# Optimization experiments

Hardware: AMD Instinct MI355X
Metric: run time of the kernel (lower is better)

The kernel has to match this reference:

```python
import jax, jax.numpy as jnp
import numpy as np
from jax import lax

B, T, D, N = 64, 4096, 256, 64


def setup_inputs() -> dict:
    key = jax.random.key(0)
    ks = jax.random.split(key, 3)
    return {
        "x": jax.random.normal(ks[0], (B, T, D), dtype=jnp.float32),
        "mask": jnp.ones((B, T), dtype=bool),
        "W": jax.random.normal(ks[1], (D, N), dtype=jnp.float32) * (1.0 / np.sqrt(D)),
        "b": jnp.zeros((N,), dtype=jnp.float32),
        "trans": jax.random.normal(ks[2], (N, N), dtype=jnp.float32) * 0.1,
        "left_boundary": jnp.zeros((N,), dtype=jnp.float32),
        "right_boundary": jnp.zeros((N,), dtype=jnp.float32),
    }


def _viterbi_decode(potentials, lens, trans):
    # potentials: [B, T, N]; lens: [B] int32; trans: [N, N]
    Tt = potentials.shape[1]

    def fwd_step(state, inp):
        pot_t, t = inp  # pot_t: [B, N], t scalar time index (1..T-1)
        scores = state[:, :, None] + trans[None, :, :]        # [B, N_prev, N_cur]
        bp = jnp.argmax(scores, axis=1).astype(jnp.int32)      # [B, N]
        new_state = pot_t + jnp.max(scores, axis=1)            # [B, N]
        valid = (t < lens)[:, None]                            # carry state past length
        return jnp.where(valid, new_state, state), bp

    pots_t = jnp.swapaxes(potentials, 0, 1)  # [T, B, N]
    final_state, bps = lax.scan(fwd_step, pots_t[0], (pots_t[1:], jnp.arange(1, Tt)))
    last_tag = jnp.argmax(final_state, axis=1).astype(jnp.int32)  # [B]

    def bwd_step(tag, inp):
        bp, t = inp  # bp: [B, N] backpointers for time t+1; t in 0..T-2
        prev = jnp.take_along_axis(bp, tag[:, None], axis=1)[:, 0]
        new_tag = jnp.where(t < lens - 1, prev, last_tag)
        return new_tag, new_tag

    _, tags = lax.scan(bwd_step, last_tag, (bps, jnp.arange(Tt - 1)), reverse=True)
    # tags: [T-1, B], position t holds decoded tag at time t
    decoded = jnp.concatenate([tags.T, last_tag[:, None]], axis=1)  # [B, T]
    return decoded


def reference(x, mask, W, b, trans, left_boundary, right_boundary):
    # projection (use_kernel=True)
    pot = jnp.einsum("btd,dn->btn", x, W) + b  # [B, T, N]
    # boundary potentials (use_boundary=True): added at fixed first/last timestep
    pot = pot.at[:, 0, :].add(left_boundary)
    pot = pot.at[:, -1, :].add(right_boundary)
    lens = jnp.sum(mask.astype(jnp.int32), axis=1)  # [B]
    decoded = _viterbi_decode(pot, lens, trans)
    return decoded, pot, lens, trans
```

## Files before the change

### kernel.cpp

```cpp
#include <hip/hip_runtime.h>

#define B_ 64
#define T_ 4096
#define D_ 256
#define N_ 64

typedef float f32x16 __attribute__((ext_vector_type(16)));

__global__ __launch_bounds__(64) void k_misc(const unsigned char* __restrict__ mask,
                                             const float* __restrict__ trans,
                                             float* __restrict__ out_lens,
                                             float* __restrict__ out_trans,
                                             int* __restrict__ lens_i) {
  int blk = blockIdx.x, lane = threadIdx.x;
  if (blk < B_) {
    int probe = (int)mask[0] + (int)mask[1] + (int)mask[2] + (int)mask[3];
    int cnt = 0;
    if (probe >= 2) {
      const unsigned char* row = mask + (size_t)blk * T_;
      for (int i = lane; i < T_; i += 64) cnt += row[i] ? 1 : 0;
    } else {
      const int* rowi = (const int*)mask + (size_t)blk * T_;
      for (int i = lane; i < T_; i += 64) cnt += rowi[i] ? 1 : 0;
    }
    #pragma unroll
    for (int off = 32; off > 0; off >>= 1) cnt += __shfl_down(cnt, off, 64);
    if (lane == 0) { out_lens[blk] = (float)cnt; lens_i[blk] = cnt; }
  } else {
    int base = (blk - B_) * 1024;
    for (int i = lane; i < 1024; i += 64) out_trans[base + i] = trans[base + i];
  }
}

__global__ __launch_bounds__(256, 4) void k_gemm(const float* __restrict__ x,
                                                 const float* __restrict__ W,
                                                 const float* __restrict__ bias,
                                                 const float* __restrict__ lb,
                                                 const float* __restrict__ rb,
                                                 float* __restrict__ pot) {
  int wave = (blockIdx.x * blockDim.x + threadIdx.x) >> 6;
  int wave_u = __builtin_amdgcn_readfirstlane(wave);
  int lane = threadIdx.x & 63;
  long row0 = (long)wave_u * 16;

  float bv = bias[lane];
  float lbv = lb[lane];
  float rbv = rb[lane];

  float acc[16];
  #pragma unroll
  for (int r = 0; r < 16; ++r) {
    int t = (int)((row0 + r) & (T_ - 1));
    float a = bv;
    if (t == 0)      a += lbv;
    if (t == T_ - 1) a += rbv;
    acc[r] = a;
  }

  const float* xb = x + (size_t)row0 * D_;

  #pragma unroll
  for (int c = 0; c < 4; ++c) {
    int d0 = c * 64;
    float w[64];
    #pragma unroll
    for (int k = 0; k < 64; ++k) w[k] = W[(d0 + k) * N_ + lane];
    #pragma unroll
    for (int r = 0; r < 16; ++r) {
      const f32x16* xr = reinterpret_cast<const f32x16*>(xb + r * D_ + d0);
      #pragma unroll
      for (int q = 0; q < 4; ++q) {
        f32x16 xv = xr[q];
        #pragma unroll
        for (int j = 0; j < 16; ++j) acc[r] += xv[j] * w[q * 16 + j];
      }
    }
  }

  #pragma unroll
  for (int r = 0; r < 16; ++r) pot[(row0 + r) * N_ + lane] = acc[r];
}

#define FWD_STEP(TIDX, PREG)                                                      \
  {                                                                               \
    float pot_t = PREG;                                                           \
    int tp = (TIDX) + 4; if (tp > T_ - 1) tp = T_ - 1;                            \
    PREG = pb[(size_t)tp * N_ + lane];                                            \
    float m[64];                                                                  \
    _Pragma("unroll")                                                             \
    for (int g = 0; g < 16; ++g) {                                                \
      float4 s4 = st4v[g];                                                        \
      float2 ca = make_float2(s4.x, s4.y) + t2[2 * g];                            \
      float2 cb = make_float2(s4.z, s4.w) + t2[2 * g + 1];                        \
      m[4 * g + 0] = ca.x; m[4 * g + 1] = ca.y;                                   \
      m[4 * g + 2] = cb.x; m[4 * g + 3] = cb.y;                                   \
    }                                                                             \
    float r1[22];                                                                 \
    _Pragma("unroll")                                                             \
    for (int i = 0; i < 21; ++i)                                                  \
      r1[i] = fmaxf(fmaxf(m[3 * i], m[3 * i + 1]), m[3 * i + 2]);                 \
    r1[21] = m[63];                                                               \
    float r2[8];                                                                  \
    _Pragma("unroll")                                                             \
    for (int i = 0; i < 7; ++i)                                                   \
      r2[i] = fmaxf(fmaxf(r1[3 * i], r1[3 * i + 1]), r1[3 * i + 2]);              \
    r2[7] = r1[21];                                                               \
    float r3a = fmaxf(fmaxf(r2[0], r2[1]), r2[2]);                                \
    float r3b = fmaxf(fmaxf(r2[3], r2[4]), r2[5]);                                \
    float r3c = fmaxf(r2[6], r2[7]);                                              \
    float best = fmaxf(fmaxf(r3a, r3b), r3c);                                     \
    float ns = pot_t + best;                                                      \
    state = ((TIDX) < len_b) ? ns : state;                                        \
    sb[(size_t)(TIDX) * N_ + lane] = state;                                       \
    __builtin_amdgcn_wave_barrier();                                              \
    st[lane] = state;                                                             \
    __builtin_amdgcn_wave_barrier();                                              \
  }

__global__ __launch_bounds__(64, 1) void k_fwd_states(const float* __restrict__ pot,
                                                      const float* __restrict__ trans,
                                                      const int* __restrict__ lens_i,
                                                      float* __restrict__ states,
                                                      float* __restrict__ fstate) {
  int b = blockIdx.x, lane = threadIdx.x;
  __shared__ float4 st4v[16];
  float* st = (float*)st4v;

  float2 t2[32];
  #pragma unroll
  for (int p = 0; p < 32; ++p)
    t2[p] = make_float2(trans[(2 * p) * N_ + lane], trans[(2 * p + 1) * N_ + lane]);

  const float* pb = pot + (size_t)b * T_ * N_;
  float* sb = states + (size_t)b * T_ * N_;
  int len_b = lens_i[b];

  float state = pb[lane];
  st[lane] = state;
  sb[lane] = state;
  __builtin_amdgcn_wave_barrier();

  float p0 = pb[1 * N_ + lane];
  float p1 = pb[2 * N_ + lane];
  float p2 = pb[3 * N_ + lane];
  float p3 = pb[4 * N_ + lane];

  int t = 1;
  for (; t + 3 <= T_ - 1; t += 4) {
    FWD_STEP(t + 0, p0);
    FWD_STEP(t + 1, p1);
    FWD_STEP(t + 2, p2);
    FWD_STEP(t + 3, p3);
  }
  FWD_STEP(t + 0, p0);
  FWD_STEP(t + 1, p1);
  FWD_STEP(t + 2, p2);

  fstate[b * N_ + lane] = state;
}

#define BP_CHUNK 64
__global__ __launch_bounds__(64, 2) void k_bp(const float* __restrict__ states,
                                              const float* __restrict__ trans,
                                              unsigned char* __restrict__ bp) {
  int nchunk = T_ / BP_CHUNK;
  int b = blockIdx.x / nchunk;
  int chunk = blockIdx.x - b * nchunk;
  int lane = threadIdx.x;

  float tcol[64];
  #pragma unroll
  for (int p = 0; p < 64; ++p) tcol[p] = trans[p * N_ + lane];

  int t0 = chunk * BP_CHUNK;
  int tstart = (t0 == 0) ? 1 : t0;
  int tend = t0 + BP_CHUNK;

  for (int t = tstart; t < tend; ++t) {
    const f32x16* sr = reinterpret_cast<const f32x16*>(states + ((size_t)b * T_ + (t - 1)) * N_);
    f32x16 s0 = sr[0], s1 = sr[1], s2 = sr[2], s3 = sr[3];

    float c[64];
    #pragma unroll
    for (int j = 0; j < 16; ++j) {
      c[j]      = s0[j] + tcol[j];
      c[16 + j] = s1[j] + tcol[16 + j];
      c[32 + j] = s2[j] + tcol[32 + j];
      c[48 + j] = s3[j] + tcol[48 + j];
    }

    float r1[22];
    #pragma unroll
    for (int i = 0; i < 21; ++i) r1[i] = fmaxf(fmaxf(c[3 * i], c[3 * i + 1]), c[3 * i + 2]);
    r1[21] = c[63];
    float r2[8];
    #pragma unroll
    for (int i = 0; i < 7; ++i) r2[i] = fmaxf(fmaxf(r1[3 * i], r1[3 * i + 1]), r1[3 * i + 2]);
    r2[7] = r1[21];
    float r3a = fmaxf(fmaxf(r2[0], r2[1]), r2[2]);
    float r3b = fmaxf(fmaxf(r2[3], r2[4]), r2[5]);
    float r3c = fmaxf(r2[6], r2[7]);
    float best = fmaxf(fmaxf(r3a, r3b), r3c);

    int bpi = 63;
    #pragma unroll
    for (int p = 62; p >= 0; --p) bpi = (c[p] == best) ? p : bpi;

    bp[((size_t)b * T_ + t) * N_ + lane] = (unsigned char)bpi;
  }
}

__global__ __launch_bounds__(64, 1) void k_bwd(const unsigned char* __restrict__ bp,
                                               const float* __restrict__ fstate,
                                               const int* __restrict__ lens_i,
                                               float* __restrict__ decoded) {
  int b = blockIdx.x, lane = threadIdx.x;

  __shared__ float fv[64];
  __shared__ int sh_tag;
  fv[lane] = fstate[b * N_ + lane];
  __syncthreads();
  if (lane == 0) {
    float best = fv[0]; int tg = 0;
    for (int i = 1; i < 64; ++i) if (fv[i] > best) { best = fv[i]; tg = i; }
    sh_tag = tg;
  }
  __syncthreads();
  int last_tag = sh_tag;
  int len_b = lens_i[b];

  const unsigned char* bpb = bp + (size_t)b * T_ * N_;
  float* dec = decoded + (size_t)b * T_;

  int tag = last_tag;
  if (lane == 0) dec[T_ - 1] = (float)last_tag;

  const int G = 16;
  int bufA[G], bufB[G];
  const int k0 = T_ - 1;
  #pragma unroll
  for (int i = 0; i < G; ++i) bufA[i] = (int)bpb[(size_t)(k0 - i) * N_ + lane];

  const int nrows = T_ - 1;
  const int groups = nrows / G;

  for (int g = 0; g < groups; ++g) {
    int kn = k0 - G * (g + 1);
    #pragma unroll
    for (int i = 0; i < G; ++i)
      bufB[i] = (kn - i >= 1) ? (int)bpb[(size_t)(kn - i) * N_ + lane] : 0;

    int kbase = k0 - G * g;
    #pragma unroll
    for (int i = 0; i < G; ++i) {
      int k = kbase - i;
      int prev = __shfl(bufA[i], tag, 64);
      int t = k - 1;
      tag = (t < len_b - 1) ? prev : last_tag;
      if (lane == 0) dec[t] = (float)tag;
    }
    #pragma unroll
    for (int i = 0; i < G; ++i) bufA[i] = bufB[i];
  }

  int kbase = k0 - G * groups;
  #pragma unroll
  for (int i = 0; i < G; ++i) {
    int k = kbase - i;
    if (k >= 1) {
      int prev = __shfl(bufA[i], tag, 64);
      int t = k - 1;
      tag = (t < len_b - 1) ? prev : last_tag;
      if (lane == 0) dec[t] = (float)tag;
    }
  }
}

extern "C" void kernel_launch(void* const* d_in, const int* in_sizes, int n_in,
                              void* d_out, int out_size, void* d_ws, size_t ws_size,
                              hipStream_t stream) {
  const float* x            = (const float*)d_in[0];
  const unsigned char* mask = (const unsigned char*)d_in[1];
  const float* W            = (const float*)d_in[2];
  const float* bias         = (const float*)d_in[3];
  const float* trans        = (const float*)d_in[4];
  const float* lb           = (const float*)d_in[5];
  const float* rb           = (const float*)d_in[6];

  float* out         = (float*)d_out;
  float* out_decoded = out;
  float* out_pot     = out + (size_t)B_ * T_;
  float* out_lens    = out_pot + (size_t)B_ * T_ * N_;
  float* out_trans   = out_lens + B_;

  const size_t bp_bytes     = (size_t)B_ * T_ * N_;
  const size_t fstate_off   = bp_bytes;
  const size_t lens_off     = fstate_off + (size_t)B_ * N_ * 4;
  const size_t states_off   = lens_off + 256;
  const size_t states_bytes = (size_t)B_ * T_ * N_ * 4;

  unsigned char* bp = (unsigned char*)d_ws;
  float* fstate     = (float*)((char*)d_ws + fstate_off);
  int*   lens_i     = (int*)((char*)d_ws + lens_off);
  float* states     = (float*)((char*)d_ws + states_off);

  k_misc<<<68, 64, 0, stream>>>(mask, trans, out_lens, out_trans, lens_i);
  k_gemm<<<(B_ * T_) / 64, 256, 0, stream>>>(x, W, bias, lb, rb, out_pot);
  k_fwd_states<<<B_, 64, 0, stream>>>(out_pot, trans, lens_i, states, fstate);
  k_bp<<<B_ * (T_ / BP_CHUNK), 64, 0, stream>>>(states, trans, bp);
  k_bwd<<<B_, 64, 0, stream>>>(bp, fstate, lens_i, out_decoded);
}
```

Before: 1.759 ms.

## Broadcast Viterbi state via readlane instead of LDS; deepen prefetch and scalarize backtrace

The forward recurrence now takes each previous-state value with readlane from the register holding it, in place of writing state to LDS and reading it back between wave barriers. This removes the per-step LDS round trip and barriers from the serial critical path, though it issues 64 readlanes per step. The pot prefetch distance grows from 4 to 8 timesteps. The backtrace holds the tag in a scalar and uses readlane instead of ds_bpermute shuffles, with a larger group of 32 buffered rows.

```diff
diff --git a/kernel.cpp b/kernel.cpp
--- a/kernel.cpp
+++ b/kernel.cpp
@@ -84,16 +84,14 @@
 #define FWD_STEP(TIDX, PREG)                                                      \
   {                                                                               \
     float pot_t = PREG;                                                           \
-    int tp = (TIDX) + 4; if (tp > T_ - 1) tp = T_ - 1;                            \
+    int tp = (TIDX) + 8; if (tp > T_ - 1) tp = T_ - 1;                            \
     PREG = pb[(size_t)tp * N_ + lane];                                            \
     float m[64];                                                                  \
     _Pragma("unroll")                                                             \
-    for (int g = 0; g < 16; ++g) {                                                \
-      float4 s4 = st4v[g];                                                        \
-      float2 ca = make_float2(s4.x, s4.y) + t2[2 * g];                            \
-      float2 cb = make_float2(s4.z, s4.w) + t2[2 * g + 1];                        \
-      m[4 * g + 0] = ca.x; m[4 * g + 1] = ca.y;                                   \
-      m[4 * g + 2] = cb.x; m[4 * g + 3] = cb.y;                                   \
+    for (int p = 0; p < 64; ++p) {                                                \
+      float sp = __int_as_float(                                                  \
+          __builtin_amdgcn_readlane(__float_as_int(state), p));                   \
+      m[p] = sp + tcol[p];                                                        \
     }                                                                             \
     float r1[22];                                                                 \
     _Pragma("unroll")                                                             \
@@ -112,9 +110,6 @@
     float ns = pot_t + best;                                                      \
     state = ((TIDX) < len_b) ? ns : state;                                        \
     sb[(size_t)(TIDX) * N_ + lane] = state;                                       \
-    __builtin_amdgcn_wave_barrier();                                              \
-    st[lane] = state;                                                             \
-    __builtin_amdgcn_wave_barrier();                                              \
   }
 
 __global__ __launch_bounds__(64, 1) void k_fwd_states(const float* __restrict__ pot,
@@ -123,38 +118,45 @@
                                                       float* __restrict__ states,
                                                       float* __restrict__ fstate) {
   int b = blockIdx.x, lane = threadIdx.x;
-  __shared__ float4 st4v[16];
-  float* st = (float*)st4v;
-
-  float2 t2[32];
-  #pragma unroll
-  for (int p = 0; p < 32; ++p)
-    t2[p] = make_float2(trans[(2 * p) * N_ + lane], trans[(2 * p + 1) * N_ + lane]);
+
+  float tcol[64];
+  #pragma unroll
+  for (int p = 0; p < 64; ++p) tcol[p] = trans[p * N_ + lane];
 
   const float* pb = pot + (size_t)b * T_ * N_;
   float* sb = states + (size_t)b * T_ * N_;
   int len_b = lens_i[b];
 
   float state = pb[lane];
-  st[lane] = state;
   sb[lane] = state;
-  __builtin_amdgcn_wave_barrier();
 
   float p0 = pb[1 * N_ + lane];
   float p1 = pb[2 * N_ + lane];
   float p2 = pb[3 * N_ + lane];
   float p3 = pb[4 * N_ + lane];
+  float p4 = pb[5 * N_ + lane];
+  float p5 = pb[6 * N_ + lane];
+  float p6 = pb[7 * N_ + lane];
+  float p7 = pb[8 * N_ + lane];
 
   int t = 1;
-  for (; t + 3 <= T_ - 1; t += 4) {
+  for (; t + 7 <= T_ - 1; t += 8) {
     FWD_STEP(t + 0, p0);
     FWD_STEP(t + 1, p1);
     FWD_STEP(t + 2, p2);
     FWD_STEP(t + 3, p3);
+    FWD_STEP(t + 4, p4);
+    FWD_STEP(t + 5, p5);
+    FWD_STEP(t + 6, p6);
+    FWD_STEP(t + 7, p7);
   }
   FWD_STEP(t + 0, p0);
   FWD_STEP(t + 1, p1);
   FWD_STEP(t + 2, p2);
+  FWD_STEP(t + 3, p3);
+  FWD_STEP(t + 4, p4);
+  FWD_STEP(t + 5, p5);
+  FWD_STEP(t + 6, p6);
 
   fstate[b * N_ + lane] = state;
 }
@@ -226,16 +228,16 @@
     sh_tag = tg;
   }
   __syncthreads();
-  int last_tag = sh_tag;
+  int s_last = __builtin_amdgcn_readfirstlane(sh_tag);
   int len_b = lens_i[b];
 
   const unsigned char* bpb = bp + (size_t)b * T_ * N_;
   float* dec = decoded + (size_t)b * T_;
 
-  int tag = last_tag;
-  if (lane == 0) dec[T_ - 1] = (float)last_tag;
-
-  const int G = 16;
+  int s_tag = s_last;
+  if (lane == 0) dec[T_ - 1] = (float)s_last;
+
+  const int G = 32;
   int bufA[G], bufB[G];
   const int k0 = T_ - 1;
   #pragma unroll
@@ -254,10 +256,10 @@
     #pragma unroll
     for (int i = 0; i < G; ++i) {
       int k = kbase - i;
-      int prev = __shfl(bufA[i], tag, 64);
+      int prev = __builtin_amdgcn_readlane(bufA[i], s_tag);
       int t = k - 1;
-      tag = (t < len_b - 1) ? prev : last_tag;
-      if (lane == 0) dec[t] = (float)tag;
+      s_tag = (t < len_b - 1) ? prev : s_last;
+      if (lane == 0) dec[t] = (float)s_tag;
     }
     #pragma unroll
     for (int i = 0; i < G; ++i) bufA[i] = bufB[i];
@@ -268,10 +270,10 @@
   for (int i = 0; i < G; ++i) {
     int k = kbase - i;
     if (k >= 1) {
-      int prev = __shfl(bufA[i], tag, 64);
+      int prev = __builtin_amdgcn_readlane(bufA[i], s_tag);
       int t = k - 1;
-      tag = (t < len_b - 1) ? prev : last_tag;
-      if (lane == 0) dec[t] = (float)tag;
+      s_tag = (t < len_b - 1) ? prev : s_last;
+      if (lane == 0) dec[t] = (float)s_tag;
     }
   }
 }
@@ -297,7 +299,6 @@
   const size_t fstate_off   = bp_bytes;
   const size_t lens_off     = fstate_off + (size_t)B_ * N_ * 4;
   const size_t states_off   = lens_off + 256;
-  const size_t states_bytes = (size_t)B_ * T_ * N_ * 4;
 
   unsigned char* bp = (unsigned char*)d_ws;
   float* fstate     = (float*)((char*)d_ws + fstate_off);
```

Result: slower. 1.933 ms (+9.9%).
